# Kernel tuning notes

Measured on AMD Instinct MI355X. Metric: run time of the kernel, lower is better.

Reference implementation:

```python
import jax, jax.numpy as jnp
from jax import lax
import numpy as np

NX, NQ, NU, B = 512, 512, 128, 32768
EPS = 1e-3
ALPHA = 0.0


def setup_inputs() -> dict:
    key = jax.random.key(0)
    ks = jax.random.split(key, 8)
    std = 1.0 / np.sqrt(NX)
    return {
        "t": jnp.zeros((1,), jnp.float32),
        "xi": jax.random.normal(ks[0], (B, NX), jnp.float32),
        "u": jax.random.normal(ks[1], (B, NU), jnp.float32),
        "Pstar": jax.random.normal(ks[2], (NX, NX), jnp.float32) * std,
        "Chi": jax.random.normal(ks[3], (NX, NQ), jnp.float32) * std,
        "Y1": jax.random.normal(ks[4], (NX, NX), jnp.float32) * std,
        "B2": jax.random.normal(ks[5], (NX, NU), jnp.float32) * std,
        "D12": jax.random.normal(ks[6], (NQ, NU), jnp.float32) * std,
        "X": jax.random.normal(ks[7], (NX + NQ, NX + NQ), jnp.float32) * std,
    }


def reference(t, xi, u, Pstar, Chi, Y1, B2, D12, X):
    # Parameter construction (direct parametrization of a contractive REN)
    P = 0.5 * (Pstar @ Pstar.T) + EPS * jnp.eye(NX, dtype=xi.dtype)
    H = X @ X.T + EPS * jnp.eye(NX + NQ, dtype=xi.dtype)
    H1 = H[:NX, :NX]          # [nx, nx]
    H2 = H[:NX, NX:]          # [nx, nq]
    H4 = H[NX:, NX:]          # [nq, nq]
    Y = -0.5 * (H1 + ALPHA * P + Y1 - Y1.T)
    lam = 0.5 * jnp.diagonal(H4)                 # Lambda = diag(lam)
    Pinv = jnp.linalg.inv(P)
    A = Pinv @ Y                                  # F.linear(inv(P), Y.T)
    D11 = -jnp.tril(H4, -1) / lam[:, None]        # strictly lower triangular
    C1 = Chi.T / lam[:, None]                     # [nq, nx]
    B1 = Pinv @ (-H2 - Chi)                       # [nx, nq]

    # Forward-substitution recurrence: w[:, i] = tanh(xi@C1[i] + w@D11[i] + u@D12[i])
    base = xi @ C1.T + u @ D12.T                  # [B, nq], bv = 0 (bias=False)

    def step(w, i):
        v = base[:, i] + w @ D11[i]               # [B]; D11[i, j>=i] == 0
        w = w.at[:, i].set(jnp.tanh(v))
        return w, None

    w0 = jnp.zeros((xi.shape[0], NQ), xi.dtype)
    w, _ = lax.scan(step, w0, jnp.arange(NQ))

    # xi_dot = A xi + B1 w + B2 u  (bx = 0 since bias=False)
    xi_ = xi @ A.T + w @ B1.T + u @ B2.T
    return xi_
```

## Files before the change

kernel.cpp:

```cpp
#include <hip/hip_runtime.h>
#include <hip/hip_bf16.h>
#include <cstdint>
#include <cstddef>

#define NXD 512
#define NQD 512
#define NUD 128
#define NBATCH 32768
#define EPSV 1e-3f
#define KBASE 640
#define KFIN 1152

typedef unsigned short u16;
typedef short bf16x8 __attribute__((ext_vector_type(8)));
typedef _Float16 f16x8 __attribute__((ext_vector_type(8)));
typedef float f32x4 __attribute__((ext_vector_type(4)));

__device__ __forceinline__ void gload_lds16(const u16* g, u16* l) {
  __builtin_amdgcn_global_load_lds((const __attribute__((address_space(1))) void*)g,
                                   (__attribute__((address_space(3))) void*)l, 16, 0, 0);
}

__device__ __forceinline__ float fast_tanh(float x) {
  float e = __expf(2.0f * x);
  return 1.0f - 2.0f / (e + 1.0f);
}

__global__ __launch_bounds__(256) void k_syrk(const float* __restrict__ A,
                                              float* __restrict__ C,
                                              int N, int K, float scale) {
  __shared__ float As[16][68];
  __shared__ float Bs[16][68];
  int tid = threadIdx.x;
  int row = tid >> 2;
  int q4 = (tid & 3) * 4;
  int tx = tid & 15, ty = tid >> 4;
  int i0 = blockIdx.x * 64, j0 = blockIdx.y * 64;
  float acc[4][4] = {};
  for (int k0 = 0; k0 < K; k0 += 16) {
    float4 a = *(const float4*)&A[(size_t)(i0 + row) * K + k0 + q4];
    float4 b = *(const float4*)&A[(size_t)(j0 + row) * K + k0 + q4];
    __syncthreads();
    As[q4 + 0][row] = a.x; As[q4 + 1][row] = a.y; As[q4 + 2][row] = a.z; As[q4 + 3][row] = a.w;
    Bs[q4 + 0][row] = b.x; Bs[q4 + 1][row] = b.y; Bs[q4 + 2][row] = b.z; Bs[q4 + 3][row] = b.w;
    __syncthreads();
#pragma unroll
    for (int kk = 0; kk < 16; ++kk) {
      float av[4], bv[4];
      *(float4*)av = *(const float4*)&As[kk][ty * 4];
      *(float4*)bv = *(const float4*)&Bs[kk][tx * 4];
#pragma unroll
      for (int i = 0; i < 4; ++i)
#pragma unroll
        for (int j = 0; j < 4; ++j) acc[i][j] += av[i] * bv[j];
    }
  }
#pragma unroll
  for (int i = 0; i < 4; ++i)
#pragma unroll
    for (int j = 0; j < 4; ++j) {
      int r = i0 + ty * 4 + i, c = j0 + tx * 4 + j;
      float v = acc[i][j] * scale;
      if (r == c) v += EPSV;
      C[(size_t)r * N + c] = v;
    }
}

__global__ void k_prep(const float* __restrict__ H, const float* __restrict__ Y1,
                       const float* __restrict__ Chi, float* __restrict__ D11,
                       float* __restrict__ C1, float* __restrict__ RHS) {
  int i = blockIdx.x;
  float lam = 0.5f * H[(size_t)(512 + i) * 1024 + 512 + i];
  float rlam = 1.0f / lam;
  for (int j = threadIdx.x; j < 512; j += blockDim.x) {
    float h4 = H[(size_t)(512 + i) * 1024 + 512 + j];
    D11[i * 512 + j] = (j < i) ? (-h4 * rlam) : 0.0f;
    C1[i * 512 + j] = Chi[(size_t)j * 512 + i] * rlam;
    float y = -0.5f * (H[(size_t)i * 1024 + j] + Y1[(size_t)i * 512 + j] - Y1[(size_t)j * 512 + i]);
    RHS[(size_t)i * 1024 + j] = y;
    RHS[(size_t)i * 1024 + 512 + j] = -H[(size_t)i * 1024 + 512 + j] - Chi[(size_t)i * 512 + j];
  }
}

__global__ __launch_bounds__(256) void k_chol_diag64(float* __restrict__ P, int kb) {
  __shared__ float colbuf[2][72];
  int tid = threadIdx.x;
  int ty = tid >> 4, tx = tid & 15;
  int base = kb * 64;
  float T[4][4];
#pragma unroll
  for (int rr = 0; rr < 4; ++rr)
#pragma unroll
    for (int cc = 0; cc < 4; ++cc)
      T[rr][cc] = P[(size_t)(base + ty * 4 + rr) * 512 + base + tx * 4 + cc];

  for (int c = 0; c < 64; ++c) {
    float* cb = colbuf[c & 1];
    if (tx == (c >> 2)) {
      int cc = c & 3;
#pragma unroll
      for (int rr = 0; rr < 4; ++rr) cb[ty * 4 + rr] = T[rr][cc];
    }
    __syncthreads();
    float dcv = cb[c];
    float dc = sqrtf(dcv);
    float rdc = 1.0f / dc;
    float rdcv = 1.0f / dcv;
    if (tx == (c >> 2)) {
      int cc = c & 3;
#pragma unroll
      for (int rr = 0; rr < 4; ++rr) {
        int r = ty * 4 + rr;
        if (r == c) T[rr][cc] = dc;
        else if (r > c) T[rr][cc] *= rdc;
      }
    }
    float cr[4], cj[4];
#pragma unroll
    for (int rr = 0; rr < 4; ++rr) {
      int r = ty * 4 + rr;
      cr[rr] = (r > c) ? cb[r] * rdcv : 0.0f;
    }
#pragma unroll
    for (int cc = 0; cc < 4; ++cc) {
      int j = tx * 4 + cc;
      cj[cc] = (j > c) ? cb[j] : 0.0f;
    }
#pragma unroll
    for (int rr = 0; rr < 4; ++rr)
#pragma unroll
      for (int cc = 0; cc < 4; ++cc) T[rr][cc] -= cr[rr] * cj[cc];
  }
  __syncthreads();
#pragma unroll
  for (int rr = 0; rr < 4; ++rr)
#pragma unroll
    for (int cc = 0; cc < 4; ++cc)
      P[(size_t)(base + ty * 4 + rr) * 512 + base + tx * 4 + cc] = T[rr][cc];
}

__global__ __launch_bounds__(256) void k_trsm64(float* __restrict__ P, int kb, int rem) {
  __shared__ float Ls[64 * 64];
  int tid = threadIdx.x;
  int base = kb * 64;
  for (int idx = tid; idx < 64 * 64; idx += 256) {
    int r = idx >> 6, c = idx & 63;
    Ls[idx] = P[(size_t)(base + r) * 512 + base + c];
  }
  __syncthreads();
  int ir = blockIdx.x * 256 + tid;
  if (ir >= rem) return;
  int i = base + 64 + ir;
  float x[64];
  float* Arow = &P[(size_t)i * 512 + base];
#pragma unroll
  for (int c = 0; c < 64; ++c) {
    float a0 = Arow[c], a1 = 0.f, a2 = 0.f, a3 = 0.f;
#pragma unroll
    for (int m = 0; m < c; m += 4) {
      a0 -= x[m] * Ls[c * 64 + m];
      if (m + 1 < c) a1 -= x[m + 1] * Ls[c * 64 + m + 1];
      if (m + 2 < c) a2 -= x[m + 2] * Ls[c * 64 + m + 2];
      if (m + 3 < c) a3 -= x[m + 3] * Ls[c * 64 + m + 3];
    }
    x[c] = ((a0 + a1) + (a2 + a3)) / Ls[c * 64 + c];
  }
#pragma unroll
  for (int c = 0; c < 64; ++c) Arow[c] = x[c];
}

__global__ __launch_bounds__(256) void k_solve_f64(const float* __restrict__ P,
                                                   float* __restrict__ W, int kb) {
  __shared__ float Ls[64 * 64];
  int tid = threadIdx.x;
  int base = kb * 64;
  int c = blockIdx.x * 256 + tid;
  for (int idx = tid; idx < 64 * 64; idx += 256) {
    int r = idx >> 6, m = idx & 63;
    Ls[idx] = P[(size_t)(base + r) * 512 + base + m];
  }
  __syncthreads();
  float z[64];
#pragma unroll
  for (int r = 0; r < 64; ++r) {
    float a0 = W[(size_t)(base + r) * 1024 + c], a1 = 0.f, a2 = 0.f, a3 = 0.f;
#pragma unroll
    for (int m = 0; m < r; m += 4) {
      a0 -= z[m] * Ls[r * 64 + m];
      if (m + 1 < r) a1 -= z[m + 1] * Ls[r * 64 + m + 1];
      if (m + 2 < r) a2 -= z[m + 2] * Ls[r * 64 + m + 2];
      if (m + 3 < r) a3 -= z[m + 3] * Ls[r * 64 + m + 3];
    }
    z[r] = ((a0 + a1) + (a2 + a3)) / Ls[r * 64 + r];
  }
#pragma unroll
  for (int r = 0; r < 64; ++r) W[(size_t)(base + r) * 1024 + c] = z[r];
}

__global__ __launch_bounds__(256) void k_solve_b64(const float* __restrict__ P,
                                                   float* __restrict__ W, int kb) {
  __shared__ float LsT[64 * 64];
  int tid = threadIdx.x;
  int base = kb * 64;
  int c = blockIdx.x * 256 + tid;
  for (int idx = tid; idx < 64 * 64; idx += 256) {
    int r = idx >> 6, m = idx & 63;
    LsT[idx] = P[(size_t)(base + m) * 512 + base + r];
  }
  __syncthreads();
  float z[64];
#pragma unroll
  for (int rr = 0; rr < 64; ++rr) {
    int r = 63 - rr;
    float a0 = W[(size_t)(base + r) * 1024 + c], a1 = 0.f, a2 = 0.f, a3 = 0.f;
#pragma unroll
    for (int m = r + 1; m < 64; m += 4) {
      a0 -= z[m] * LsT[r * 64 + m];
      if (m + 1 < 64) a1 -= z[m + 1] * LsT[r * 64 + m + 1];
      if (m + 2 < 64) a2 -= z[m + 2] * LsT[r * 64 + m + 2];
      if (m + 3 < 64) a3 -= z[m + 3] * LsT[r * 64 + m + 3];
    }
    z[r] = ((a0 + a1) + (a2 + a3)) / LsT[r * 64 + r];
  }
#pragma unroll
  for (int r = 0; r < 64; ++r) W[(size_t)(base + r) * 1024 + c] = z[r];
}

template <int TA, int TB>
__global__ __launch_bounds__(256) void k_gemm_acc(float* __restrict__ C, int ldc,
                                                  int ci0, int cj0,
                                                  const float* __restrict__ A, int lda, int ai0,
                                                  const float* __restrict__ B, int ldb, int bj0,
                                                  int k0, int K) {
  __shared__ float As[16][68];
  __shared__ float Bs[16][68];
  int tid = threadIdx.x;
  int tx = tid & 15, ty = tid >> 4;
  int i0 = blockIdx.x * 64, j0 = blockIdx.y * 64;
  float acc[4][4] = {};
  for (int kc = 0; kc < K; kc += 16) {
    float4 av, bv;
    if (TA == 0) {
      int row = tid >> 2, q4 = (tid & 3) * 4;
      av = *(const float4*)&A[(size_t)(ai0 + i0 + row) * lda + k0 + kc + q4];
    } else {
      int kr = tid >> 4, m4 = (tid & 15) * 4;
      av = *(const float4*)&A[(size_t)(k0 + kc + kr) * lda + ai0 + i0 + m4];
    }
    if (TB == 0) {
      int kr = tid >> 4, j4 = (tid & 15) * 4;
      bv = *(const float4*)&B[(size_t)(k0 + kc + kr) * ldb + bj0 + j0 + j4];
    } else {
      int row = tid >> 2, q4 = (tid & 3) * 4;
      bv = *(const float4*)&B[(size_t)(bj0 + j0 + row) * ldb + k0 + kc + q4];
    }
    __syncthreads();
    if (TA == 0) {
      int row = tid >> 2, q4 = (tid & 3) * 4;
      As[q4 + 0][row] = av.x; As[q4 + 1][row] = av.y; As[q4 + 2][row] = av.z; As[q4 + 3][row] = av.w;
    } else {
      int kr = tid >> 4, m4 = (tid & 15) * 4;
      *(float4*)&As[kr][m4] = av;
    }
    if (TB == 0) {
      int kr = tid >> 4, j4 = (tid & 15) * 4;
      *(float4*)&Bs[kr][j4] = bv;
    } else {
      int row = tid >> 2, q4 = (tid & 3) * 4;
      Bs[q4 + 0][row] = bv.x; Bs[q4 + 1][row] = bv.y; Bs[q4 + 2][row] = bv.z; Bs[q4 + 3][row] = bv.w;
    }
    __syncthreads();
#pragma unroll
    for (int kk = 0; kk < 16; ++kk) {
      float a4[4], b4[4];
      *(float4*)a4 = *(const float4*)&As[kk][ty * 4];
      *(float4*)b4 = *(const float4*)&Bs[kk][tx * 4];
#pragma unroll
      for (int i = 0; i < 4; ++i)
#pragma unroll
        for (int j = 0; j < 4; ++j) acc[i][j] += a4[i] * b4[j];
    }
  }
#pragma unroll
  for (int i = 0; i < 4; ++i)
#pragma unroll
    for (int j = 0; j < 4; ++j)
      C[(size_t)(ci0 + i0 + ty * 4 + i) * ldc + cj0 + j0 + tx * 4 + j] -= acc[i][j];
}

__global__ __launch_bounds__(256) void k_pack_z(const float* __restrict__ xi,
                                                const float* __restrict__ u,
                                                __hip_bfloat16* __restrict__ Zb) {
  size_t b = blockIdx.x;
  for (int c = threadIdx.x; c < KBASE; c += 256) {
    float v = (c < 512) ? xi[b * 512 + c] : u[b * 128 + (c - 512)];
    Zb[b * KFIN + c] = __float2bfloat16(v);
  }
}

__global__ __launch_bounds__(256) void k_pack_w(const float* __restrict__ C1,
                                                const float* __restrict__ D12,
                                                const float* __restrict__ Wm,
                                                const float* __restrict__ B2,
                                                const float* __restrict__ D11,
                                                __hip_bfloat16* __restrict__ Wbase,
                                                __hip_bfloat16* __restrict__ Wfin,
                                                u16* __restrict__ D11h) {
  int n = blockIdx.x;
  for (int c = threadIdx.x; c < KBASE; c += 256) {
    float v = (c < 512) ? C1[(size_t)n * 512 + c] : D12[(size_t)n * 128 + (c - 512)];
    Wbase[(size_t)n * KBASE + c] = __float2bfloat16(v);
  }
  for (int c = threadIdx.x; c < KFIN; c += 256) {
    float v;
    if (c < 512) v = Wm[(size_t)n * 1024 + c];
    else if (c < 640) v = B2[(size_t)n * 128 + (c - 512)];
    else v = Wm[(size_t)n * 1024 + 512 + (c - 640)];
    Wfin[(size_t)n * KFIN + c] = __float2bfloat16(v);
  }
  for (int c = threadIdx.x; c < 512; c += 256) {
    _Float16 h = (_Float16)D11[(size_t)n * 512 + c];
    D11h[(size_t)n * 512 + c] = *(u16*)&h;
  }
}

__global__ __launch_bounds__(256) void k_gemm_bf16(
    const u16* __restrict__ Z, int ldz,
    const u16* __restrict__ W, int ldw,
    float* __restrict__ C, int N, int K) {
  __shared__ u16 As[128 * 32];
  __shared__ u16 Bs[128 * 32];
  int tid = threadIdx.x;
  int l = tid & 63, wv = tid >> 6;
  size_t m0 = (size_t)blockIdx.x * 128;
  int n0 = blockIdx.y * 128;

  int ra = wv * 16 + (l >> 2);
  int gq = (l & 3) ^ ((l >> 2) & 3) ^ (l >> 4);
  const u16* ga0 = Z + (m0 + ra) * (size_t)ldz + gq * 8;
  const u16* ga1 = Z + (m0 + ra + 64) * (size_t)ldz + gq * 8;
  const u16* gb0 = W + (size_t)(n0 + ra) * ldw + gq * 8;
  const u16* gb1 = W + (size_t)(n0 + ra + 64) * ldw + gq * 8;
  u16* la0 = &As[wv * 512];
  u16* la1 = &As[2048 + wv * 512];
  u16* lb0 = &Bs[wv * 512];
  u16* lb1 = &Bs[2048 + wv * 512];

  int wm = (wv & 1) * 64, wn = (wv >> 1) * 64;
  int fr = l & 15;
  int fs = (l >> 4) ^ (l & 3) ^ ((l >> 2) & 3);
  int offa[4], offb[4];
#pragma unroll
  for (int t = 0; t < 4; ++t) {
    offa[t] = (wm + t * 16 + fr) * 32 + fs * 8;
    offb[t] = (wn + t * 16 + fr) * 32 + fs * 8;
  }

  f32x4 acc[4][4] = {};
  for (int k0 = 0; k0 < K; k0 += 32) {
    __syncthreads();
    gload_lds16(ga0, la0);
    gload_lds16(ga1, la1);
    gload_lds16(gb0, lb0);
    gload_lds16(gb1, lb1);
    ga0 += 32; ga1 += 32; gb0 += 32; gb1 += 32;
    __syncthreads();
    bf16x8 af[4], bfr[4];
#pragma unroll
    for (int t = 0; t < 4; ++t) {
      af[t] = *(const bf16x8*)&As[offa[t]];
      bfr[t] = *(const bf16x8*)&Bs[offb[t]];
    }
#pragma unroll
    for (int mt = 0; mt < 4; ++mt)
#pragma unroll
      for (int nt = 0; nt < 4; ++nt)
        acc[mt][nt] = __builtin_amdgcn_mfma_f32_16x16x32_bf16(af[mt], bfr[nt], acc[mt][nt], 0, 0, 0);
  }

#pragma unroll
  for (int mt = 0; mt < 4; ++mt)
#pragma unroll
    for (int nt = 0; nt < 4; ++nt) {
      int ncol = n0 + wn + nt * 16 + (l & 15);
#pragma unroll
      for (int r = 0; r < 4; ++r) {
        size_t mrow = m0 + wm + mt * 16 + (l >> 4) * 4 + r;
        C[mrow * N + ncol] = acc[mt][nt][r];
      }
    }
}

#define WSTR 520
__global__ __launch_bounds__(256) void k_scan_mfma(
    const float* __restrict__ basep,
    const float* __restrict__ D11,
    const u16* __restrict__ D11h,
    u16* __restrict__ zw) {
  __shared__ u16 wbf_s[4][16 * WSTR];
  __shared__ float ptr_s[4][16 * 16];
  __shared__ float dls_s[4][16 * 16];

  int tid = threadIdx.x;
  int wv = tid >> 6, l = tid & 63;
  int r = l & 15;
  int q = l >> 4;
  size_t gm0 = (size_t)blockIdx.x * 64 + wv * 16;

  u16* wbf = wbf_s[wv];
  float* ptr = ptr_s[wv];
  float* dls = dls_s[wv];

  float wreg[4] = {0.f, 0.f, 0.f, 0.f};

  for (int c = 0; c < 32; ++c) {
    int i0 = c * 16;
    int nk = i0 >> 5;
    int rem = c & 1;
    const u16* drow = &D11h[(size_t)(i0 + r) * 512 + q * 8];
    f16x8 bfr[16];
#pragma unroll
    for (int k = 0; k < 16; ++k)
      if (k < nk) bfr[k] = *(const f16x8*)&drow[k * 32];
    f16x8 brem = {};
    if (rem && q < 2) brem = *(const f16x8*)&drow[nk * 32];
#pragma unroll
    for (int k = 0; k < 4; ++k) {
      int ii = q + 4 * k;
      dls[ii * 16 + r] = D11[(size_t)(i0 + ii) * 512 + i0 + r];
    }
    f32x4 acc = {0.f, 0.f, 0.f, 0.f};
#pragma unroll
    for (int k = 0; k < 16; ++k)
      if (k < nk) {
        f16x8 a = *(const f16x8*)&wbf[r * WSTR + k * 32 + q * 8];
        acc = __builtin_amdgcn_mfma_f32_16x16x32_f16(a, bfr[k], acc, 0, 0, 0);
      }
    if (rem) {
      f16x8 a = {};
      if (q < 2) a = *(const f16x8*)&wbf[r * WSTR + nk * 32 + q * 8];
      acc = __builtin_amdgcn_mfma_f32_16x16x32_f16(a, brem, acc, 0, 0, 0);
    }
#pragma unroll
    for (int reg = 0; reg < 4; ++reg)
      acc[reg] += basep[(gm0 + q * 4 + reg) * 512 + i0 + r];
#pragma unroll
    for (int reg = 0; reg < 4; ++reg) {
      int m = q * 4 + reg;
      int nsw = r ^ ((m & 3) << 2);
      ptr[m * 16 + nsw] = acc[reg];
    }
    float p[16];
#pragma unroll
    for (int j = 0; j < 4; ++j) {
      float4 v4 = *(const float4*)&ptr[r * 16 + j * 4];
      int cj = (j ^ (r & 3)) * 4;
      p[cj + 0] = v4.x; p[cj + 1] = v4.y; p[cj + 2] = v4.z; p[cj + 3] = v4.w;
    }
#pragma unroll
    for (int s = 0; s < 16; ++s) {
      float prod = 0.f;
#pragma unroll
      for (int m = 0; m < 4; ++m)
        prod = fmaf(wreg[m], dls[s * 16 + q + 4 * m], prod);
      prod += __shfl_xor(prod, 16);
      prod += __shfl_xor(prod, 32);
      float w = fast_tanh(p[s] + prod);
      if ((s & 3) == q) {
        wreg[s >> 2] = w;
        *(_Float16*)&wbf[r * WSTR + i0 + s] = (_Float16)w;
      }
    }
  }
#pragma unroll
  for (int it = 0; it < 16; ++it) {
    int idx = it * 64 + l;
    int row = idx >> 6;
    int ch = idx & 63;
    f16x8 v = *(const f16x8*)&wbf[row * WSTR + ch * 8];
    u16 o[8];
#pragma unroll
    for (int e = 0; e < 8; ++e) {
      __hip_bfloat16 b = __float2bfloat16((float)v[e]);
      o[e] = *(u16*)&b;
    }
    *(uint4*)&zw[(gm0 + row) * KFIN + ch * 8] = *(const uint4*)o;
  }
}

extern "C" void kernel_launch(void* const* d_in, const int* in_sizes, int n_in,
                              void* d_out, int out_size, void* d_ws, size_t ws_size,
                              hipStream_t stream) {
  const float* xi = (const float*)d_in[1];
  const float* u = (const float*)d_in[2];
  const float* Pstar = (const float*)d_in[3];
  const float* Chi = (const float*)d_in[4];
  const float* Y1 = (const float*)d_in[5];
  const float* B2 = (const float*)d_in[6];
  const float* D12 = (const float*)d_in[7];
  const float* X = (const float*)d_in[8];
  float* out = (float*)d_out;

  char* ws = (char*)d_ws;
  __hip_bfloat16* Zb = (__hip_bfloat16*)ws;
  size_t off = (size_t)NBATCH * KFIN * sizeof(__hip_bfloat16);
  float* H = (float*)(ws + off);    off += (size_t)1024 * 1024 * 4;
  float* Pm = (float*)(ws + off);   off += (size_t)512 * 512 * 4;
  float* D11 = (float*)(ws + off);  off += (size_t)512 * 512 * 4;
  float* C1 = (float*)(ws + off);   off += (size_t)512 * 512 * 4;
  float* Wm = (float*)(ws + off);   off += (size_t)512 * 1024 * 4;
  __hip_bfloat16* Wbase = (__hip_bfloat16*)(ws + off); off += (size_t)512 * KBASE * 2;
  __hip_bfloat16* Wfin = (__hip_bfloat16*)(ws + off);  off += (size_t)512 * KFIN * 2;
  u16* D11h = (u16*)(ws + off);                        off += (size_t)512 * 512 * 2;

  k_pack_z<<<NBATCH, 256, 0, stream>>>(xi, u, Zb);

  k_syrk<<<dim3(16, 16), 256, 0, stream>>>(X, H, 1024, 1024, 1.0f);
  k_syrk<<<dim3(8, 8), 256, 0, stream>>>(Pstar, Pm, 512, 512, 0.5f);
  k_prep<<<512, 256, 0, stream>>>(H, Y1, Chi, D11, C1, Wm);

  for (int kb = 0; kb < 8; ++kb) {
    k_chol_diag64<<<1, 256, 0, stream>>>(Pm, kb);
    int rem = 512 - (kb + 1) * 64;
    if (rem > 0) {
      k_trsm64<<<(rem + 255) / 256, 256, 0, stream>>>(Pm, kb, rem);
      k_gemm_acc<0, 1><<<dim3(rem / 64, rem / 64), 256, 0, stream>>>(
          Pm, 512, (kb + 1) * 64, (kb + 1) * 64,
          Pm, 512, (kb + 1) * 64,
          Pm, 512, (kb + 1) * 64, kb * 64, 64);
    }
  }
  for (int kb = 0; kb < 8; ++kb) {
    k_solve_f64<<<4, 256, 0, stream>>>(Pm, Wm, kb);
    int rem = 512 - (kb + 1) * 64;
    if (rem > 0)
      k_gemm_acc<0, 0><<<dim3(rem / 64, 16), 256, 0, stream>>>(
          Wm, 1024, (kb + 1) * 64, 0,
          Pm, 512, (kb + 1) * 64,
          Wm, 1024, 0, kb * 64, 64);
  }
  for (int kb = 7; kb >= 0; --kb) {
    k_solve_b64<<<4, 256, 0, stream>>>(Pm, Wm, kb);
    if (kb > 0)
      k_gemm_acc<1, 0><<<dim3(kb, 16), 256, 0, stream>>>(
          Wm, 1024, 0, 0,
          Pm, 512, 0,
          Wm, 1024, 0, kb * 64, 64);
  }

  k_pack_w<<<512, 256, 0, stream>>>(C1, D12, Wm, B2, D11, Wbase, Wfin, D11h);

  k_gemm_bf16<<<dim3(NBATCH / 128, NQD / 128), 256, 0, stream>>>(
      (const u16*)Zb, KFIN, (const u16*)Wbase, KBASE, out, NQD, KBASE);
  k_scan_mfma<<<NBATCH / 64, 256, 0, stream>>>(out, D11, D11h, (u16*)(Zb + KBASE));
  k_gemm_bf16<<<dim3(NBATCH / 128, NXD / 128), 256, 0, stream>>>(
      (const u16*)Zb, KFIN, (const u16*)Wfin, KFIN, out, NXD, KFIN);
}
```

Before: 1.611 ms.

## Fuse parameter construction and Cholesky solves into one persistent grid-synced kernel

Replaces the roughly 50 small kernel launches for SYRK, prep, blocked Cholesky, triangular solves and weight packing with a single persistent 256-block kernel that uses atomic grid barriers. The triangular solves are reformulated as an explicit blocked inverse of the Cholesky factor, built by recursive doubling, followed by two dense GEMMs. This is meant to remove launch overhead and the serialized per-column solve kernels. In exchange it relies on all 256 blocks being co-resident for the spin barriers, and the inverse-based solve may change numerics slightly.

```diff
diff --git a/kernel.cpp b/kernel.cpp
--- a/kernel.cpp
+++ b/kernel.cpp
@@ -26,64 +26,71 @@
   return 1.0f - 2.0f / (e + 1.0f);
 }
 
-__global__ __launch_bounds__(256) void k_syrk(const float* __restrict__ A,
-                                              float* __restrict__ C,
-                                              int N, int K, float scale) {
-  __shared__ float As[16][68];
-  __shared__ float Bs[16][68];
+__device__ __forceinline__ void gbar(unsigned int* bar, unsigned int target) {
+  __syncthreads();
+  if (threadIdx.x == 0) {
+    __hip_atomic_fetch_add(bar, 1u, __ATOMIC_RELEASE, __HIP_MEMORY_SCOPE_AGENT);
+    while (__hip_atomic_load(bar, __ATOMIC_ACQUIRE, __HIP_MEMORY_SCOPE_AGENT) < target)
+      __builtin_amdgcn_s_sleep(2);
+  }
+  __syncthreads();
+}
+
+template <int TA, int TB>
+__device__ __forceinline__ void tile_mm(float acc[4][4], float* As, float* Bs,
+                                        const float* A, int lda, int ai0, int ak0,
+                                        const float* B, int ldb, int bj0, int bk0,
+                                        int K) {
   int tid = threadIdx.x;
-  int row = tid >> 2;
-  int q4 = (tid & 3) * 4;
   int tx = tid & 15, ty = tid >> 4;
-  int i0 = blockIdx.x * 64, j0 = blockIdx.y * 64;
-  float acc[4][4] = {};
-  for (int k0 = 0; k0 < K; k0 += 16) {
-    float4 a = *(const float4*)&A[(size_t)(i0 + row) * K + k0 + q4];
-    float4 b = *(const float4*)&A[(size_t)(j0 + row) * K + k0 + q4];
+  for (int kc = 0; kc < K; kc += 16) {
+    float4 av, bv;
+    if (TA == 0) {
+      int row = tid >> 2, q4 = (tid & 3) * 4;
+      av = *(const float4*)&A[(size_t)(ai0 + row) * lda + ak0 + kc + q4];
+    } else {
+      int kr = tid >> 4, m4 = (tid & 15) * 4;
+      av = *(const float4*)&A[(size_t)(ak0 + kc + kr) * lda + ai0 + m4];
+    }
+    if (TB == 0) {
+      int kr = tid >> 4, j4 = (tid & 15) * 4;
+      bv = *(const float4*)&B[(size_t)(bk0 + kc + kr) * ldb + bj0 + j4];
+    } else {
+      int row = tid >> 2, q4 = (tid & 3) * 4;
+      bv = *(const float4*)&B[(size_t)(bj0 + row) * ldb + bk0 + kc + q4];
+    }
     __syncthreads();
-    As[q4 + 0][row] = a.x; As[q4 + 1][row] = a.y; As[q4 + 2][row] = a.z; As[q4 + 3][row] = a.w;
-    Bs[q4 + 0][row] = b.x; Bs[q4 + 1][row] = b.y; Bs[q4 + 2][row] = b.z; Bs[q4 + 3][row] = b.w;
+    if (TA == 0) {
+      int row = tid >> 2, q4 = (tid & 3) * 4;
+      As[(q4 + 0) * 68 + row] = av.x; As[(q4 + 1) * 68 + row] = av.y;
+      As[(q4 + 2) * 68 + row] = av.z; As[(q4 + 3) * 68 + row] = av.w;
+    } else {
+      int kr = tid >> 4, m4 = (tid & 15) * 4;
+      *(float4*)&As[kr * 68 + m4] = av;
+    }
+    if (TB == 0) {
+      int kr = tid >> 4, j4 = (tid & 15) * 4;
+      *(float4*)&Bs[kr * 68 + j4] = bv;
+    } else {
+      int row = tid >> 2, q4 = (tid & 3) * 4;
+      Bs[(q4 + 0) * 68 + row] = bv.x; Bs[(q4 + 1) * 68 + row] = bv.y;
+      Bs[(q4 + 2) * 68 + row] = bv.z; Bs[(q4 + 3) * 68 + row] = bv.w;
+    }
     __syncthreads();
 #pragma unroll
     for (int kk = 0; kk < 16; ++kk) {
-      float av[4], bv[4];
-      *(float4*)av = *(const float4*)&As[kk][ty * 4];
-      *(float4*)bv = *(const float4*)&Bs[kk][tx * 4];
+      float a4[4], b4[4];
+      *(float4*)a4 = *(const float4*)&As[kk * 68 + ty * 4];
+      *(float4*)b4 = *(const float4*)&Bs[kk * 68 + tx * 4];
 #pragma unroll
       for (int i = 0; i < 4; ++i)
 #pragma unroll
-        for (int j = 0; j < 4; ++j) acc[i][j] += av[i] * bv[j];
-    }
-  }
-#pragma unroll
-  for (int i = 0; i < 4; ++i)
-#pragma unroll
-    for (int j = 0; j < 4; ++j) {
-      int r = i0 + ty * 4 + i, c = j0 + tx * 4 + j;
-      float v = acc[i][j] * scale;
-      if (r == c) v += EPSV;
-      C[(size_t)r * N + c] = v;
-    }
-}
-
-__global__ void k_prep(const float* __restrict__ H, const float* __restrict__ Y1,
-                       const float* __restrict__ Chi, float* __restrict__ D11,
-                       float* __restrict__ C1, float* __restrict__ RHS) {
-  int i = blockIdx.x;
-  float lam = 0.5f * H[(size_t)(512 + i) * 1024 + 512 + i];
-  float rlam = 1.0f / lam;
-  for (int j = threadIdx.x; j < 512; j += blockDim.x) {
-    float h4 = H[(size_t)(512 + i) * 1024 + 512 + j];
-    D11[i * 512 + j] = (j < i) ? (-h4 * rlam) : 0.0f;
-    C1[i * 512 + j] = Chi[(size_t)j * 512 + i] * rlam;
-    float y = -0.5f * (H[(size_t)i * 1024 + j] + Y1[(size_t)i * 512 + j] - Y1[(size_t)j * 512 + i]);
-    RHS[(size_t)i * 1024 + j] = y;
-    RHS[(size_t)i * 1024 + 512 + j] = -H[(size_t)i * 1024 + 512 + j] - Chi[(size_t)i * 512 + j];
-  }
-}
-
-__global__ __launch_bounds__(256) void k_chol_diag64(float* __restrict__ P, int kb) {
-  __shared__ float colbuf[2][72];
+        for (int j = 0; j < 4; ++j) acc[i][j] += a4[i] * b4[j];
+    }
+  }
+}
+
+__device__ void chol_diag64(float* Pm, int kb, float* cb2, float* Ls) {
   int tid = threadIdx.x;
   int ty = tid >> 4, tx = tid & 15;
   int base = kb * 64;
@@ -92,10 +99,10 @@
   for (int rr = 0; rr < 4; ++rr)
 #pragma unroll
     for (int cc = 0; cc < 4; ++cc)
-      T[rr][cc] = P[(size_t)(base + ty * 4 + rr) * 512 + base + tx * 4 + cc];
+      T[rr][cc] = Pm[(size_t)(base + ty * 4 + rr) * 512 + base + tx * 4 + cc];
 
   for (int c = 0; c < 64; ++c) {
-    float* cb = colbuf[c & 1];
+    float* cb = cb2 + (c & 1) * 72;
     if (tx == (c >> 2)) {
       int cc = c & 3;
 #pragma unroll
@@ -135,157 +142,246 @@
 #pragma unroll
   for (int rr = 0; rr < 4; ++rr)
 #pragma unroll
-    for (int cc = 0; cc < 4; ++cc)
-      P[(size_t)(base + ty * 4 + rr) * 512 + base + tx * 4 + cc] = T[rr][cc];
-}
-
-__global__ __launch_bounds__(256) void k_trsm64(float* __restrict__ P, int kb, int rem) {
-  __shared__ float Ls[64 * 64];
+    for (int cc = 0; cc < 4; ++cc) {
+      float v = T[rr][cc];
+      Pm[(size_t)(base + ty * 4 + rr) * 512 + base + tx * 4 + cc] = v;
+      Ls[(ty * 4 + rr) * 64 + tx * 4 + cc] = v;
+    }
+  __syncthreads();
+}
+
+__device__ void diag_inv64(const float* Pm, float* Tinv, int kb, float* Ls, float* Xs) {
   int tid = threadIdx.x;
   int base = kb * 64;
-  for (int idx = tid; idx < 64 * 64; idx += 256) {
-    int r = idx >> 6, c = idx & 63;
-    Ls[idx] = P[(size_t)(base + r) * 512 + base + c];
-  }
-  __syncthreads();
-  int ir = blockIdx.x * 256 + tid;
-  if (ir >= rem) return;
-  int i = base + 64 + ir;
-  float x[64];
-  float* Arow = &P[(size_t)i * 512 + base];
-#pragma unroll
-  for (int c = 0; c < 64; ++c) {
-    float a0 = Arow[c], a1 = 0.f, a2 = 0.f, a3 = 0.f;
-#pragma unroll
-    for (int m = 0; m < c; m += 4) {
-      a0 -= x[m] * Ls[c * 64 + m];
-      if (m + 1 < c) a1 -= x[m + 1] * Ls[c * 64 + m + 1];
-      if (m + 2 < c) a2 -= x[m + 2] * Ls[c * 64 + m + 2];
-      if (m + 3 < c) a3 -= x[m + 3] * Ls[c * 64 + m + 3];
-    }
-    x[c] = ((a0 + a1) + (a2 + a3)) / Ls[c * 64 + c];
-  }
-#pragma unroll
-  for (int c = 0; c < 64; ++c) Arow[c] = x[c];
-}
-
-__global__ __launch_bounds__(256) void k_solve_f64(const float* __restrict__ P,
-                                                   float* __restrict__ W, int kb) {
-  __shared__ float Ls[64 * 64];
+  for (int idx = tid; idx < 4096; idx += 256) {
+    Ls[idx] = Pm[(size_t)(base + (idx >> 6)) * 512 + base + (idx & 63)];
+    Xs[idx] = 0.0f;
+  }
+  __syncthreads();
+  if (tid < 64) {
+    int j = tid;
+    Xs[j * 64 + j] = 1.0f / Ls[j * 64 + j];
+    for (int i = j + 1; i < 64; ++i) {
+      float s = 0.0f;
+      for (int k = j; k < i; ++k) s += Ls[i * 64 + k] * Xs[k * 64 + j];
+      Xs[i * 64 + j] = -s / Ls[i * 64 + i];
+    }
+  }
+  __syncthreads();
+  for (int idx = tid; idx < 4096; idx += 256)
+    Tinv[(size_t)(base + (idx >> 6)) * 512 + base + (idx & 63)] = Xs[idx];
+  __syncthreads();
+}
+
+__global__ __launch_bounds__(256) void k_small(
+    const float* __restrict__ X, const float* __restrict__ Pstar,
+    const float* __restrict__ Y1, const float* __restrict__ Chi,
+    const float* __restrict__ B2, const float* __restrict__ D12,
+    float* __restrict__ H, float* __restrict__ Pm,
+    float* __restrict__ D11, float* __restrict__ C1, float* __restrict__ Wm,
+    __hip_bfloat16* __restrict__ Wbase, __hip_bfloat16* __restrict__ Wfin,
+    u16* __restrict__ D11h, unsigned int* bar) {
+  __shared__ float smem[8192];
+  float* As = smem;
+  float* Bs = smem + 1088;
+  int bid = blockIdx.x;
   int tid = threadIdx.x;
-  int base = kb * 64;
-  int c = blockIdx.x * 256 + tid;
-  for (int idx = tid; idx < 64 * 64; idx += 256) {
-    int r = idx >> 6, m = idx & 63;
-    Ls[idx] = P[(size_t)(base + r) * 512 + base + m];
-  }
-  __syncthreads();
-  float z[64];
-#pragma unroll
-  for (int r = 0; r < 64; ++r) {
-    float a0 = W[(size_t)(base + r) * 1024 + c], a1 = 0.f, a2 = 0.f, a3 = 0.f;
-#pragma unroll
-    for (int m = 0; m < r; m += 4) {
-      a0 -= z[m] * Ls[r * 64 + m];
-      if (m + 1 < r) a1 -= z[m + 1] * Ls[r * 64 + m + 1];
-      if (m + 2 < r) a2 -= z[m + 2] * Ls[r * 64 + m + 2];
-      if (m + 3 < r) a3 -= z[m + 3] * Ls[r * 64 + m + 3];
-    }
-    z[r] = ((a0 + a1) + (a2 + a3)) / Ls[r * 64 + r];
-  }
-#pragma unroll
-  for (int r = 0; r < 64; ++r) W[(size_t)(base + r) * 1024 + c] = z[r];
-}
-
-__global__ __launch_bounds__(256) void k_solve_b64(const float* __restrict__ P,
-                                                   float* __restrict__ W, int kb) {
-  __shared__ float LsT[64 * 64];
-  int tid = threadIdx.x;
-  int base = kb * 64;
-  int c = blockIdx.x * 256 + tid;
-  for (int idx = tid; idx < 64 * 64; idx += 256) {
-    int r = idx >> 6, m = idx & 63;
-    LsT[idx] = P[(size_t)(base + m) * 512 + base + r];
-  }
-  __syncthreads();
-  float z[64];
-#pragma unroll
-  for (int rr = 0; rr < 64; ++rr) {
-    int r = 63 - rr;
-    float a0 = W[(size_t)(base + r) * 1024 + c], a1 = 0.f, a2 = 0.f, a3 = 0.f;
-#pragma unroll
-    for (int m = r + 1; m < 64; m += 4) {
-      a0 -= z[m] * LsT[r * 64 + m];
-      if (m + 1 < 64) a1 -= z[m + 1] * LsT[r * 64 + m + 1];
-      if (m + 2 < 64) a2 -= z[m + 2] * LsT[r * 64 + m + 2];
-      if (m + 3 < 64) a3 -= z[m + 3] * LsT[r * 64 + m + 3];
-    }
-    z[r] = ((a0 + a1) + (a2 + a3)) / LsT[r * 64 + r];
-  }
-#pragma unroll
-  for (int r = 0; r < 64; ++r) W[(size_t)(base + r) * 1024 + c] = z[r];
-}
-
-template <int TA, int TB>
-__global__ __launch_bounds__(256) void k_gemm_acc(float* __restrict__ C, int ldc,
-                                                  int ci0, int cj0,
-                                                  const float* __restrict__ A, int lda, int ai0,
-                                                  const float* __restrict__ B, int ldb, int bj0,
-                                                  int k0, int K) {
-  __shared__ float As[16][68];
-  __shared__ float Bs[16][68];
-  int tid = threadIdx.x;
-  int tx = tid & 15, ty = tid >> 4;
-  int i0 = blockIdx.x * 64, j0 = blockIdx.y * 64;
-  float acc[4][4] = {};
-  for (int kc = 0; kc < K; kc += 16) {
-    float4 av, bv;
-    if (TA == 0) {
-      int row = tid >> 2, q4 = (tid & 3) * 4;
-      av = *(const float4*)&A[(size_t)(ai0 + i0 + row) * lda + k0 + kc + q4];
-    } else {
-      int kr = tid >> 4, m4 = (tid & 15) * 4;
-      av = *(const float4*)&A[(size_t)(k0 + kc + kr) * lda + ai0 + i0 + m4];
-    }
-    if (TB == 0) {
-      int kr = tid >> 4, j4 = (tid & 15) * 4;
-      bv = *(const float4*)&B[(size_t)(k0 + kc + kr) * ldb + bj0 + j0 + j4];
-    } else {
-      int row = tid >> 2, q4 = (tid & 3) * 4;
-      bv = *(const float4*)&B[(size_t)(bj0 + j0 + row) * ldb + k0 + kc + q4];
-    }
-    __syncthreads();
-    if (TA == 0) {
-      int row = tid >> 2, q4 = (tid & 3) * 4;
-      As[q4 + 0][row] = av.x; As[q4 + 1][row] = av.y; As[q4 + 2][row] = av.z; As[q4 + 3][row] = av.w;
-    } else {
-      int kr = tid >> 4, m4 = (tid & 15) * 4;
-      *(float4*)&As[kr][m4] = av;
-    }
-    if (TB == 0) {
-      int kr = tid >> 4, j4 = (tid & 15) * 4;
-      *(float4*)&Bs[kr][j4] = bv;
-    } else {
-      int row = tid >> 2, q4 = (tid & 3) * 4;
-      Bs[q4 + 0][row] = bv.x; Bs[q4 + 1][row] = bv.y; Bs[q4 + 2][row] = bv.z; Bs[q4 + 3][row] = bv.w;
-    }
-    __syncthreads();
-#pragma unroll
-    for (int kk = 0; kk < 16; ++kk) {
-      float a4[4], b4[4];
-      *(float4*)a4 = *(const float4*)&As[kk][ty * 4];
-      *(float4*)b4 = *(const float4*)&Bs[kk][tx * 4];
+  unsigned int bcnt = 0;
+
+  float* Z1 = H;
+  float* Tinv = H + 524288;
+  float* Tbuf = H + 786432;
+
+  {
+    int bi = bid >> 4, bj = bid & 15;
+    float acc[4][4] = {};
+    tile_mm<0, 1>(acc, As, Bs, X, 1024, bi * 64, 0, X, 1024, bj * 64, 0, 1024);
+    int tx = tid & 15, ty = tid >> 4;
+#pragma unroll
+    for (int i = 0; i < 4; ++i)
+#pragma unroll
+      for (int j = 0; j < 4; ++j) {
+        int r = bi * 64 + ty * 4 + i, c2 = bj * 64 + tx * 4 + j;
+        float v = acc[i][j];
+        if (r == c2) v += EPSV;
+        H[(size_t)r * 1024 + c2] = v;
+      }
+  }
+  if (bid < 36) {
+    int pi = 0, r2 = bid;
+    while (r2 > pi) { r2 -= pi + 1; ++pi; }
+    int pj = r2;
+    float acc[4][4] = {};
+    tile_mm<0, 1>(acc, As, Bs, Pstar, 512, pi * 64, 0, Pstar, 512, pj * 64, 0, 512);
+    int tx = tid & 15, ty = tid >> 4;
+#pragma unroll
+    for (int i = 0; i < 4; ++i)
+#pragma unroll
+      for (int j = 0; j < 4; ++j) {
+        int r = pi * 64 + ty * 4 + i, c2 = pj * 64 + tx * 4 + j;
+        float v = 0.5f * acc[i][j];
+        if (r == c2) v += EPSV;
+        Pm[(size_t)r * 512 + c2] = v;
+      }
+  }
+  gbar(bar, (++bcnt) * 256u);
+
+#pragma unroll
+  for (int rr = 0; rr < 2; ++rr) {
+    int i = bid * 2 + rr;
+    float lam = 0.5f * H[(size_t)(512 + i) * 1024 + 512 + i];
+    float rlam = 1.0f / lam;
+    for (int j = tid; j < 512; j += 256) {
+      float h4 = H[(size_t)(512 + i) * 1024 + 512 + j];
+      D11[i * 512 + j] = (j < i) ? (-h4 * rlam) : 0.0f;
+      C1[i * 512 + j] = Chi[(size_t)j * 512 + i] * rlam;
+      float y = -0.5f * (H[(size_t)i * 1024 + j] + Y1[(size_t)i * 512 + j] - Y1[(size_t)j * 512 + i]);
+      Wm[(size_t)i * 1024 + j] = y;
+      Wm[(size_t)i * 1024 + 512 + j] = -H[(size_t)i * 1024 + 512 + j] - Chi[(size_t)i * 512 + j];
+    }
+  }
+  gbar(bar, (++bcnt) * 256u);
+
+  for (int kb = 0; kb < 8; ++kb) {
+    if (bid == 0) {
+      chol_diag64(Pm, kb, smem + 4096, smem);
+      int rem = 512 - (kb + 1) * 64;
+      float* Ls = smem;
+      for (int ch = 0; ch < rem; ch += 256) {
+        int ir = ch + tid;
+        if (ir < rem) {
+          int i = (kb + 1) * 64 + ir;
+          float x[64];
+          float* Arow = &Pm[(size_t)i * 512 + kb * 64];
+#pragma unroll
+          for (int c = 0; c < 64; ++c) {
+            float a0 = Arow[c], a1 = 0.f, a2 = 0.f, a3 = 0.f;
+#pragma unroll
+            for (int m = 0; m < c; m += 4) {
+              a0 -= x[m] * Ls[c * 64 + m];
+              if (m + 1 < c) a1 -= x[m + 1] * Ls[c * 64 + m + 1];
+              if (m + 2 < c) a2 -= x[m + 2] * Ls[c * 64 + m + 2];
+              if (m + 3 < c) a3 -= x[m + 3] * Ls[c * 64 + m + 3];
+            }
+            x[c] = ((a0 + a1) + (a2 + a3)) / Ls[c * 64 + c];
+          }
+#pragma unroll
+          for (int c = 0; c < 64; ++c) Arow[c] = x[c];
+        }
+      }
+    } else if (bid == 1 && kb > 0) {
+      diag_inv64(Pm, Tinv, kb - 1, smem, smem + 4096);
+    } else if (kb == 0 && bid >= 2) {
+      for (int idx = (bid - 2) * 256 + tid; idx < 262144; idx += 254 * 256)
+        Tinv[idx] = 0.0f;
+    }
+    gbar(bar, (++bcnt) * 256u);
+
+    int nr2 = 7 - kb;
+    int count = nr2 * (nr2 + 1) / 2;
+    if (bid < count) {
+      int i = 0, r2 = bid;
+      while (r2 > i) { r2 -= i + 1; ++i; }
+      int j = r2;
+      int p1 = (kb + 1) * 64;
+      float acc[4][4] = {};
+      tile_mm<0, 1>(acc, As, Bs, Pm, 512, p1 + i * 64, kb * 64,
+                    Pm, 512, p1 + j * 64, kb * 64, 64);
+      int tx = tid & 15, ty = tid >> 4;
+#pragma unroll
+      for (int ii = 0; ii < 4; ++ii)
+#pragma unroll
+        for (int jj = 0; jj < 4; ++jj)
+          Pm[(size_t)(p1 + i * 64 + ty * 4 + ii) * 512 + p1 + j * 64 + tx * 4 + jj] -= acc[ii][jj];
+    } else if (kb == 7 && bid == 0) {
+      diag_inv64(Pm, Tinv, 7, smem, smem + 4096);
+    }
+    gbar(bar, (++bcnt) * 256u);
+  }
+
+  for (int l = 0; l < 3; ++l) {
+    int s = 64 << l, sd = s >> 6, tpp = sd * sd;
+    int ntil = (4 >> l) * tpp;
+    int p = 0, ti = 0, tj = 0;
+    if (bid < ntil) {
+      p = bid / tpp;
+      int t = bid % tpp;
+      ti = t / sd;
+      tj = t % sd;
+    }
+    int C0 = 2 * p * s, R0 = C0 + s;
+    float* Tb = Tbuf + p * s * s;
+    if (bid < ntil) {
+      float acc[4][4] = {};
+      tile_mm<0, 0>(acc, As, Bs, Pm, 512, R0 + ti * 64, C0,
+                    Tinv, 512, C0 + tj * 64, C0, s);
+      int tx = tid & 15, ty = tid >> 4;
 #pragma unroll
       for (int i = 0; i < 4; ++i)
 #pragma unroll
-        for (int j = 0; j < 4; ++j) acc[i][j] += a4[i] * b4[j];
-    }
-  }
-#pragma unroll
-  for (int i = 0; i < 4; ++i)
-#pragma unroll
-    for (int j = 0; j < 4; ++j)
-      C[(size_t)(ci0 + i0 + ty * 4 + i) * ldc + cj0 + j0 + tx * 4 + j] -= acc[i][j];
+        for (int j = 0; j < 4; ++j)
+          Tb[(size_t)(ti * 64 + ty * 4 + i) * s + tj * 64 + tx * 4 + j] = acc[i][j];
+    }
+    gbar(bar, (++bcnt) * 256u);
+    if (bid < ntil) {
+      float acc[4][4] = {};
+      tile_mm<0, 0>(acc, As, Bs, Tinv, 512, R0 + ti * 64, R0,
+                    Tb, s, tj * 64, 0, s);
+      int tx = tid & 15, ty = tid >> 4;
+#pragma unroll
+      for (int i = 0; i < 4; ++i)
+#pragma unroll
+        for (int j = 0; j < 4; ++j)
+          Tinv[(size_t)(R0 + ti * 64 + ty * 4 + i) * 512 + C0 + tj * 64 + tx * 4 + j] = -acc[i][j];
+    }
+    gbar(bar, (++bcnt) * 256u);
+  }
+
+  {
+    int ti = bid >> 4, tj = bid & 15;
+    if (bid < 128) {
+      float acc[4][4] = {};
+      tile_mm<0, 0>(acc, As, Bs, Tinv, 512, ti * 64, 0, Wm, 1024, tj * 64, 0, 512);
+      int tx = tid & 15, ty = tid >> 4;
+#pragma unroll
+      for (int i = 0; i < 4; ++i)
+#pragma unroll
+        for (int j = 0; j < 4; ++j)
+          Z1[(size_t)(ti * 64 + ty * 4 + i) * 1024 + tj * 64 + tx * 4 + j] = acc[i][j];
+    }
+    gbar(bar, (++bcnt) * 256u);
+    if (bid < 128) {
+      float acc[4][4] = {};
+      tile_mm<1, 0>(acc, As, Bs, Tinv, 512, ti * 64, 0, Z1, 1024, tj * 64, 0, 512);
+      int tx = tid & 15, ty = tid >> 4;
+#pragma unroll
+      for (int i = 0; i < 4; ++i)
+#pragma unroll
+        for (int j = 0; j < 4; ++j)
+          Wm[(size_t)(ti * 64 + ty * 4 + i) * 1024 + tj * 64 + tx * 4 + j] = acc[i][j];
+    }
+    gbar(bar, (++bcnt) * 256u);
+  }
+
+#pragma unroll
+  for (int rr = 0; rr < 2; ++rr) {
+    int n = bid * 2 + rr;
+    for (int c = tid; c < KBASE; c += 256) {
+      float v = (c < 512) ? C1[(size_t)n * 512 + c] : D12[(size_t)n * 128 + (c - 512)];
+      Wbase[(size_t)n * KBASE + c] = __float2bfloat16(v);
+    }
+    for (int c = tid; c < KFIN; c += 256) {
+      float v;
+      if (c < 512) v = Wm[(size_t)n * 1024 + c];
+      else if (c < 640) v = B2[(size_t)n * 128 + (c - 512)];
+      else v = Wm[(size_t)n * 1024 + 512 + (c - 640)];
+      Wfin[(size_t)n * KFIN + c] = __float2bfloat16(v);
+    }
+    for (int c = tid; c < 512; c += 256) {
+      _Float16 h = (_Float16)D11[(size_t)n * 512 + c];
+      D11h[(size_t)n * 512 + c] = *(u16*)&h;
+    }
+  }
 }
 
 __global__ __launch_bounds__(256) void k_pack_z(const float* __restrict__ xi,
@@ -295,32 +391,6 @@
   for (int c = threadIdx.x; c < KBASE; c += 256) {
     float v = (c < 512) ? xi[b * 512 + c] : u[b * 128 + (c - 512)];
     Zb[b * KFIN + c] = __float2bfloat16(v);
-  }
-}
-
-__global__ __launch_bounds__(256) void k_pack_w(const float* __restrict__ C1,
-                                                const float* __restrict__ D12,
-                                                const float* __restrict__ Wm,
-                                                const float* __restrict__ B2,
-                                                const float* __restrict__ D11,
-                                                __hip_bfloat16* __restrict__ Wbase,
-                                                __hip_bfloat16* __restrict__ Wfin,
-                                                u16* __restrict__ D11h) {
-  int n = blockIdx.x;
-  for (int c = threadIdx.x; c < KBASE; c += 256) {
-    float v = (c < 512) ? C1[(size_t)n * 512 + c] : D12[(size_t)n * 128 + (c - 512)];
-    Wbase[(size_t)n * KBASE + c] = __float2bfloat16(v);
-  }
-  for (int c = threadIdx.x; c < KFIN; c += 256) {
-    float v;
-    if (c < 512) v = Wm[(size_t)n * 1024 + c];
-    else if (c < 640) v = B2[(size_t)n * 128 + (c - 512)];
-    else v = Wm[(size_t)n * 1024 + 512 + (c - 640)];
-    Wfin[(size_t)n * KFIN + c] = __float2bfloat16(v);
-  }
-  for (int c = threadIdx.x; c < 512; c += 256) {
-    _Float16 h = (_Float16)D11[(size_t)n * 512 + c];
-    D11h[(size_t)n * 512 + c] = *(u16*)&h;
   }
 }
 
@@ -512,43 +582,14 @@
   __hip_bfloat16* Wbase = (__hip_bfloat16*)(ws + off); off += (size_t)512 * KBASE * 2;
   __hip_bfloat16* Wfin = (__hip_bfloat16*)(ws + off);  off += (size_t)512 * KFIN * 2;
   u16* D11h = (u16*)(ws + off);                        off += (size_t)512 * 512 * 2;
+  unsigned int* bar = (unsigned int*)(ws + off);       off += 256;
+
+  hipMemsetAsync(bar, 0, 256, stream);
 
   k_pack_z<<<NBATCH, 256, 0, stream>>>(xi, u, Zb);
 
-  k_syrk<<<dim3(16, 16), 256, 0, stream>>>(X, H, 1024, 1024, 1.0f);
-  k_syrk<<<dim3(8, 8), 256, 0, stream>>>(Pstar, Pm, 512, 512, 0.5f);
-  k_prep<<<512, 256, 0, stream>>>(H, Y1, Chi, D11, C1, Wm);
-
-  for (int kb = 0; kb < 8; ++kb) {
-    k_chol_diag64<<<1, 256, 0, stream>>>(Pm, kb);
-    int rem = 512 - (kb + 1) * 64;
-    if (rem > 0) {
-      k_trsm64<<<(rem + 255) / 256, 256, 0, stream>>>(Pm, kb, rem);
-      k_gemm_acc<0, 1><<<dim3(rem / 64, rem / 64), 256, 0, stream>>>(
-          Pm, 512, (kb + 1) * 64, (kb + 1) * 64,
-          Pm, 512, (kb + 1) * 64,
-          Pm, 512, (kb + 1) * 64, kb * 64, 64);
-    }
-  }
-  for (int kb = 0; kb < 8; ++kb) {
-    k_solve_f64<<<4, 256, 0, stream>>>(Pm, Wm, kb);
-    int rem = 512 - (kb + 1) * 64;
-    if (rem > 0)
-      k_gemm_acc<0, 0><<<dim3(rem / 64, 16), 256, 0, stream>>>(
-          Wm, 1024, (kb + 1) * 64, 0,
-          Pm, 512, (kb + 1) * 64,
-          Wm, 1024, 0, kb * 64, 64);
-  }
-  for (int kb = 7; kb >= 0; --kb) {
-    k_solve_b64<<<4, 256, 0, stream>>>(Pm, Wm, kb);
-    if (kb > 0)
-      k_gemm_acc<1, 0><<<dim3(kb, 16), 256, 0, stream>>>(
-          Wm, 1024, 0, 0,
-          Pm, 512, 0,
-          Wm, 1024, 0, kb * 64, 64);
-  }
-
-  k_pack_w<<<512, 256, 0, stream>>>(C1, D12, Wm, B2, D11, Wbase, Wfin, D11h);
+  k_small<<<256, 256, 0, stream>>>(X, Pstar, Y1, Chi, B2, D12, H, Pm,
+                                   D11, C1, Wm, Wbase, Wfin, D11h, bar);
 
   k_gemm_bf16<<<dim3(NBATCH / 128, NQD / 128), 256, 0, stream>>>(
       (const u16*)Zb, KFIN, (const u16*)Wbase, KBASE, out, NQD, KBASE);
```

Measured after the change: 2.055 ms. 1.28x slower.
